# Kernel optimization log

Hardware: AMD Instinct MI355X
Metric: run time of the kernel (lower is better)

## Reference

```python
import jax, jax.numpy as jnp
import numpy as np

B, T, D, H = 2, 2048, 1024, 16
Dh = D // H


def _rope(q, k):
    # q, k: (B, H, T, Dh), interleaved even/odd rotation
    t = q.shape[2]
    dh = q.shape[3]
    inv_freq = 1.0 / (10000.0 ** (jnp.arange(0, dh, 2, dtype=jnp.float32) / dh))
    pos = jnp.arange(t, dtype=jnp.float32)
    freqs = pos[:, None] * inv_freq[None, :]          # (T, Dh/2)
    sin = jnp.sin(freqs)[None, None]                  # (1,1,T,Dh/2)
    cos = jnp.cos(freqs)[None, None]

    def rot(x):
        xe, xo = x[..., ::2], x[..., 1::2]
        re = xe * cos - xo * sin
        ro = xe * sin + xo * cos
        return jnp.stack([re, ro], axis=-1).reshape(x.shape)

    return rot(q), rot(k)


def setup_inputs() -> dict:
    key = jax.random.key(0)
    k1, k2, k3 = jax.random.split(key, 3)
    s = 1.0 / np.sqrt(D)
    return {
        "x": jax.random.normal(k1, (B, T, D), dtype=jnp.float32),
        "w_qkv": jax.random.normal(k2, (3 * D, D), dtype=jnp.float32) * s,
        "b_qkv": jnp.zeros((3 * D,), dtype=jnp.float32),
        "w_out": jax.random.normal(k3, (D, D), dtype=jnp.float32) * s,
        "b_out": jnp.zeros((D,), dtype=jnp.float32),
    }


def reference(x, w_qkv, b_qkv, w_out, b_out):
    b, t, d = x.shape
    qkv = x @ w_qkv.T + b_qkv                         # (B,T,3D)
    q, k, v = jnp.split(qkv, 3, axis=-1)
    q = q.reshape(b, t, H, Dh).transpose(0, 2, 1, 3)  # (B,H,T,Dh)
    k = k.reshape(b, t, H, Dh).transpose(0, 2, 1, 3)
    v = v.reshape(b, t, H, Dh).transpose(0, 2, 1, 3)
    q, k = _rope(q, k)
    scores = jnp.einsum("bhtd,bhsd->bhts", q, k) / jnp.sqrt(jnp.float32(Dh))
    causal = jnp.tril(jnp.ones((t, t), dtype=bool))[None, None]
    scores = jnp.where(causal, scores, -jnp.inf)
    probs = jax.nn.softmax(scores, axis=-1)
    out = jnp.einsum("bhts,bhsd->bhtd", probs, v)     # (B,H,T,Dh)
    out = out.transpose(0, 2, 1, 3).reshape(b, t, d)
    return out @ w_out.T + b_out
```

## Files before the change

kernel.cpp:

```cpp
#include <hip/hip_runtime.h>
#include <hip/hip_bf16.h>
#include <math.h>
#include <type_traits>

#define B_ 2
#define T_ 2048
#define D_ 1024
#define H_ 16
#define DH_ 64

typedef __bf16 bf16_t;
typedef bf16_t bf16x8 __attribute__((ext_vector_type(8)));
typedef bf16_t bf16x4 __attribute__((ext_vector_type(4)));
typedef float f32x4 __attribute__((ext_vector_type(4)));

typedef __attribute__((address_space(1))) const void gas_void;
typedef __attribute__((address_space(3))) void las_void;

__device__ __forceinline__ void gld16(const void* g, void* l) {
    __builtin_amdgcn_global_load_lds((gas_void*)g, (las_void*)l, 16, 0, 0);
}

#define BARRIER() do { asm volatile("" ::: "memory"); __builtin_amdgcn_s_barrier(); asm volatile("" ::: "memory"); } while (0)

__global__ __launch_bounds__(256) void cvt3(const float* __restrict__ a,
                                            const float* __restrict__ b,
                                            const float* __restrict__ c,
                                            bf16_t* __restrict__ oa,
                                            bf16_t* __restrict__ ob,
                                            bf16_t* __restrict__ oc) {
    int i = blockIdx.x * 256 + threadIdx.x;
    const float* src; bf16_t* dst; int off;
    if (i < 1048576)      { src = a; dst = oa; off = i; }
    else if (i < 1835008) { src = b; dst = ob; off = i - 1048576; }
    else                  { src = c; dst = oc; off = i - 1835008; }
    float4 f = ((const float4*)src)[off];
    bf16x4 v = { (bf16_t)f.x, (bf16_t)f.y, (bf16_t)f.z, (bf16_t)f.w };
    ((bf16x4*)dst)[off] = v;
}

__global__ __launch_bounds__(256) void rope_tab_k(float2* __restrict__ tab) {
    int i = blockIdx.x * 256 + threadIdx.x;
    int t = i >> 5, d2 = i & 31;
    float invf = exp2f(-(float)d2 * 0.4152410118609203f);
    float ang = (float)t * invf;
    float sn, cs;
    sincosf(ang, &sn, &cs);
    tab[i] = make_float2(cs, sn);
}

__global__ __launch_bounds__(512, 1) void gemm256qkv(const bf16_t* __restrict__ A,
                                                     const bf16_t* __restrict__ Bw,
                                                     const float* __restrict__ bias,
                                                     const float2* __restrict__ tab,
                                                     bf16_t* __restrict__ q_out,
                                                     bf16_t* __restrict__ k_out,
                                                     bf16_t* __restrict__ vt_out) {
    __shared__ __align__(16) char smem[131072];

    int tid = threadIdx.x;
    int lane = tid & 63, wid = tid >> 6;
    int wm = wid >> 2, wn = wid & 3;
    int lr = lane & 15, lk = lane >> 4;

    int l = blockIdx.y * 12 + blockIdx.x;
    int x = l & 7, c = l >> 3;
    int by = x * 2 + (c >= 12);
    int bx = (c >= 12) ? c - 12 : c;

    f32x4 acc[8][4];
    f32x4 z = {0.f, 0.f, 0.f, 0.f};
#pragma unroll
    for (int i = 0; i < 8; i++)
#pragma unroll
        for (int j = 0; j < 4; j++) acc[i][j] = z;

    int colb = (tid * 16) & 127;
    int rb = tid >> 3;
    int csw = colb ^ ((rb & 7) << 4);
    const char* gA = (const char*)A + (size_t)(by * 256 + rb) * 2048 + csw;
    const char* gB = (const char*)Bw + (size_t)(bx * 256 + rb) * 2048 + csw;

    auto stgA = [&](int par, int h, int kt) __attribute__((always_inline)) {
        char* d = smem + par * 32768 + h * 16384;
        const char* g = gA + (size_t)h * 262144 + kt * 128;
        gld16(g, d + tid * 16);
        gld16(g + 131072, d + 8192 + tid * 16);
    };
    auto stgB = [&](int par, int h, int kt) __attribute__((always_inline)) {
        char* d = smem + 65536 + par * 32768 + h * 16384;
        const char* g = gB + (size_t)h * 262144 + kt * 128;
        gld16(g, d + tid * 16);
        gld16(g + 131072, d + 8192 + tid * 16);
    };

    int swz = (lr & 7) << 4;
    int ca0 = (lk * 16) ^ swz;
    int ca1 = (64 + lk * 16) ^ swz;

    bf16x8 Af[2][2], Bf[4][2];
    auto rdB = [&](const char* cB) __attribute__((always_inline)) {
        const char* base = cB + (wn >> 1) * 16384 + ((wn & 1) * 64) * 128 + lr * 128;
#pragma unroll
        for (int n = 0; n < 4; n++) {
            Bf[n][0] = *(const bf16x8*)(base + n * 2048 + ca0);
            Bf[n][1] = *(const bf16x8*)(base + n * 2048 + ca1);
        }
    };
    auto rdA = [&](const char* cA, int mp) __attribute__((always_inline)) {
        const char* base = cA + wm * 16384 + lr * 128;
#pragma unroll
        for (int mm = 0; mm < 2; mm++) {
            Af[mm][0] = *(const bf16x8*)(base + (mp * 2 + mm) * 2048 + ca0);
            Af[mm][1] = *(const bf16x8*)(base + (mp * 2 + mm) * 2048 + ca1);
        }
    };
    auto mfmaset = [&](int q) __attribute__((always_inline)) {
        __builtin_amdgcn_s_setprio(1);
#pragma unroll
        for (int mm = 0; mm < 2; mm++)
#pragma unroll
            for (int n = 0; n < 4; n++)
#pragma unroll
                for (int ks = 0; ks < 2; ks++)
                    acc[q * 2 + mm][n] = __builtin_amdgcn_mfma_f32_16x16x32_bf16(
                        Af[mm][ks], Bf[n][ks], acc[q * 2 + mm][n], 0, 0, 0);
        __builtin_amdgcn_s_setprio(0);
    };

    stgA(0, 0, 0); stgA(0, 1, 0); stgB(0, 0, 0); stgB(0, 1, 0);

    for (int kt = 0; kt < 15; ++kt) {
        int p = kt & 1, np = p ^ 1;
        const char* cA = smem + p * 32768;
        const char* cB = smem + 65536 + p * 32768;
        stgA(np, 0, kt + 1);
        asm volatile("s_waitcnt vmcnt(2)" ::: "memory");
        BARRIER();
        rdB(cB); rdA(cA, 0); stgA(np, 1, kt + 1);
        BARRIER(); mfmaset(0); BARRIER();
        rdA(cA, 1); stgB(np, 0, kt + 1);
        BARRIER(); mfmaset(1); BARRIER();
        rdA(cA, 2); stgB(np, 1, kt + 1);
        BARRIER(); mfmaset(2); BARRIER();
        rdA(cA, 3);
        BARRIER(); mfmaset(3); BARRIER();
    }
    {
        const char* cA = smem + 32768;
        const char* cB = smem + 65536 + 32768;
        asm volatile("s_waitcnt vmcnt(0)" ::: "memory");
        BARRIER();
        rdB(cB); rdA(cA, 0); BARRIER(); mfmaset(0); BARRIER();
        rdA(cA, 1); BARRIER(); mfmaset(1); BARRIER();
        rdA(cA, 2); BARRIER(); mfmaset(2); BARRIER();
        rdA(cA, 3); BARRIER(); mfmaset(3); BARRIER();
    }

    int m_base = by * 256 + wm * 128;
    int n_base = bx * 256 + wn * 64;
    char* myL = smem + wid * 16384;
    int which = n_base >> 10;
    int h = (n_base & 1023) >> 6;
    int b = m_base >> 11, t0 = m_base & 2047;
    int bh = b * H_ + h;
    if (which == 2) {
#pragma unroll
        for (int m = 0; m < 8; m++)
#pragma unroll
            for (int n = 0; n < 4; n++) {
                int rd = n * 16 + lr;
                float bv = bias[n_base + rd];
#pragma unroll
                for (int j = 0; j < 4; j++) {
                    int ct = m * 16 + lk * 4 + j;
                    int ct2 = (ct & 96) | (((ct >> 2) & 3) << 3) | (((ct >> 4) & 1) << 2) | (ct & 3);
                    int addr = (rd * 256 + ct2 * 2) ^ ((rd & 7) << 4);
                    *(bf16_t*)(myL + addr) = (bf16_t)(acc[m][n][j] + bv);
                }
            }
#pragma unroll
        for (int it = 0; it < 16; it++) {
            int row = it * 4 + (lane >> 4);
            int byt = (lane & 15) * 16;
            bf16x8 val = *(const bf16x8*)(myL + ((row * 256 + byt) ^ ((row & 7) << 4)));
            *(bf16x8*)(vt_out + ((size_t)bh * DH_ + row) * T_ + t0 + (lane & 15) * 8) = val;
        }
    } else {
        bf16_t* dst = which ? k_out : q_out;
        float qscl = which ? 1.0f : 0.18033688011112042f;
#pragma unroll
        for (int m = 0; m < 8; m++)
#pragma unroll
            for (int n = 0; n < 4; n++) {
                int dh = n * 16 + lr;
                float bv = bias[n_base + dh];
                int dh2 = dh >> 1;
                bool even = (dh & 1) == 0;
#pragma unroll
                for (int j = 0; j < 4; j++) {
                    int rt = m * 16 + lk * 4 + j;
                    float v = acc[m][n][j] + bv;
                    float pp = __shfl_xor(v, 1);
                    float2 cs = tab[(t0 + rt) * 32 + dh2];
                    float r = even ? v * cs.x - pp * cs.y : v * cs.x + pp * cs.y;
                    r *= qscl;
                    int addr = (rt * 128 + dh * 2) ^ ((rt & 7) << 4);
                    *(bf16_t*)(myL + addr) = (bf16_t)r;
                }
            }
#pragma unroll
        for (int it = 0; it < 16; it++) {
            int row = it * 8 + (lane >> 3);
            int byt = (lane & 7) * 16;
            bf16x8 val = *(const bf16x8*)(myL + ((row * 128 + byt) ^ ((row & 7) << 4)));
            *(bf16x8*)(dst + ((size_t)bh * T_ + t0 + row) * DH_ + (lane & 7) * 8) = val;
        }
    }
}

__global__ __launch_bounds__(256) void gemm128o(const bf16_t* __restrict__ A,
                                                const bf16_t* __restrict__ Bw,
                                                const float* __restrict__ bias,
                                                float* __restrict__ f_out,
                                                int K, int N) {
    __shared__ __align__(16) char smem[49152];
    char* b0 = smem;
    char* b1 = smem + 16384;
    char* b2 = smem + 32768;

    int tid = threadIdx.x;
    int lane = tid & 63, wid = tid >> 6;
    int wr = wid >> 1, wc = wid & 1;
    int lr = lane & 15, lk = lane >> 4;

    int l = blockIdx.y * gridDim.x + blockIdx.x;
    int chunk = (gridDim.x * gridDim.y) >> 3;
    int u = (l & 7) * chunk + (l >> 3);
    int bx = u % gridDim.x;
    int by = u / gridDim.x;

    f32x4 acc[4][4];
    f32x4 z = {0.f, 0.f, 0.f, 0.f};
#pragma unroll
    for (int i = 0; i < 4; i++)
#pragma unroll
        for (int j = 0; j < 4; j++) acc[i][j] = z;

    const char* Ab = (const char*)(A + (size_t)by * 128 * K);
    const char* Bb = (const char*)(Bw + (size_t)bx * 128 * K);
    const int rowstride = K * 2;

    int p0 = tid * 16;
    int p1 = 4096 + tid * 16;
    int r0 = p0 >> 6, r1 = p1 >> 6;
    int cb0 = (p0 & 63) ^ (((r0 >> 1) & 3) << 4);
    int cb1 = (p1 & 63) ^ (((r1 >> 1) & 3) << 4);
    size_t gA0 = (size_t)r0 * rowstride + cb0;
    size_t gA1 = (size_t)r1 * rowstride + cb1;

    int oa[4], ob[4];
#pragma unroll
    for (int m = 0; m < 4; m++) {
        int row = wr * 64 + m * 16 + lr;
        oa[m] = row * 64 + ((lk * 16) ^ (((row >> 1) & 3) << 4));
    }
#pragma unroll
    for (int n = 0; n < 4; n++) {
        int row = wc * 64 + n * 16 + lr;
        ob[n] = row * 64 + ((lk * 16) ^ (((row >> 1) & 3) << 4));
    }

    auto stg = [&](char* buf, int ks) __attribute__((always_inline)) {
        const char* Ag = Ab + (size_t)ks * 64;
        const char* Bg = Bb + (size_t)ks * 64;
        gld16(Ag + gA0, buf + p0);
        gld16(Ag + gA1, buf + p1);
        gld16(Bg + gA0, buf + 8192 + p0);
        gld16(Bg + gA1, buf + 8192 + p1);
    };

    auto iterf = [&](auto vmc, char* buf, int ks, bool dostage) __attribute__((always_inline)) {
        constexpr int VM = decltype(vmc)::value;
        if constexpr (VM == 8)      asm volatile("s_waitcnt vmcnt(8)" ::: "memory");
        else if constexpr (VM == 4) asm volatile("s_waitcnt vmcnt(4)" ::: "memory");
        else                        asm volatile("s_waitcnt vmcnt(0)" ::: "memory");
        __builtin_amdgcn_s_barrier();
        asm volatile("" ::: "memory");
        bf16x8 Af[4], Bf[4];
#pragma unroll
        for (int m = 0; m < 4; m++) Af[m] = *(const bf16x8*)(buf + oa[m]);
#pragma unroll
        for (int n = 0; n < 4; n++) Bf[n] = *(const bf16x8*)(buf + 8192 + ob[n]);
#pragma unroll
        for (int m = 0; m < 4; m++)
#pragma unroll
            for (int n = 0; n < 4; n++)
                acc[m][n] = __builtin_amdgcn_mfma_f32_16x16x32_bf16(Af[m], Bf[n], acc[m][n], 0, 0, 0);
        asm volatile("" ::: "memory");
        __builtin_amdgcn_s_barrier();
        asm volatile("" ::: "memory");
        if (dostage) stg(buf, ks);
    };

    std::integral_constant<int, 8> c8;
    std::integral_constant<int, 4> c4;
    std::integral_constant<int, 0> c0;

    stg(b0, 0);
    stg(b1, 1);
    stg(b2, 2);
    for (int s = 0; s < 30; s += 3) {
        iterf(c8, b0, s + 3, s + 3 < 32);
        iterf(c8, b1, s + 4, s + 4 < 32);
        iterf(c8, b2, s + 5, s + 5 < 32);
    }
    iterf(c4, b0, 0, false);
    iterf(c0, b1, 0, false);

    int m_base = by * 128 + wr * 64;
    int n_base = bx * 128 + wc * 64;
#pragma unroll
    for (int m = 0; m < 4; m++) {
        int gm0 = m_base + m * 16 + lk * 4;
#pragma unroll
        for (int n = 0; n < 4; n++) {
            int nc = n_base + n * 16 + lr;
            float bv = bias[nc];
#pragma unroll
            for (int j = 0; j < 4; j++)
                f_out[(size_t)(gm0 + j) * N + nc] = acc[m][n][j] + bv;
        }
    }
}

__global__ __launch_bounds__(256, 4) void attn64(const bf16_t* __restrict__ Q,
                                                 const bf16_t* __restrict__ K,
                                                 const bf16_t* __restrict__ Vt,
                                                 bf16_t* __restrict__ Ao) {
    __shared__ __align__(16) char smem[40960];

    int tid = threadIdx.x;
    int lane = tid & 63, wid = tid >> 6;
    int lr = lane & 15, lk = lane >> 4;
    int xcd = blockIdx.x & 7, idx = blockIdx.x >> 3;
    int bh = xcd * 4 + (idx & 3);
    int i5 = idx >> 2;
    int qq = i5 & 7, rr = i5 >> 3;
    int qt = (rr == 0) ? qq : (rr == 1) ? 15 - qq : (rr == 2) ? 16 + qq : 31 - qq;
    int q0 = qt * 64;
    int qrel = wid * 16 + lr;

    const bf16_t* Qp = Q + ((size_t)bh * T_ + q0 + qrel) * DH_;
    bf16x8 qf0 = *(const bf16x8*)(Qp + lk * 8);
    bf16x8 qf1 = *(const bf16x8*)(Qp + 32 + lk * 8);

    f32x4 zz = {0.f, 0.f, 0.f, 0.f};
    f32x4 oacc[4];
#pragma unroll
    for (int dt = 0; dt < 4; dt++) oacc[dt] = zz;
    float mrun = -__builtin_inff(), lsum = 0.f;

    const char* Kbase = (const char*)(K + (size_t)bh * T_ * DH_);
    const char* Vbase = (const char*)(Vt + (size_t)bh * DH_ * T_);

    auto stage = [&](int s, char* Kd, char* Vd) __attribute__((always_inline)) {
        int kv0 = s * 64;
        const char* Kg = Kbase + (size_t)kv0 * 128;
#pragma unroll
        for (int c = 0; c < 2; c++) {
            int o = c * 4096 + tid * 16;
            int r = o >> 7;
            int g = o ^ ((r & 7) << 4);
            gld16(Kg + g, Kd + o);
            gld16(Vbase + (size_t)r * (T_ * 2) + kv0 * 2 + (g & 127), Vd + o);
        }
    };

    float p[4][4];
    bf16x8 pb0, pb1;

    auto do_qk = [&](const char* Kc, auto dmc) __attribute__((always_inline)) {
        constexpr bool DM = decltype(dmc)::value;
#pragma unroll
        for (int kt = 0; kt < 4; kt++) {
            int row = kt * 16 + lr;
            int key = (row & 7) << 4;
            bf16x8 kf0 = *(const bf16x8*)(Kc + ((row * 128 + lk * 16) ^ key));
            bf16x8 kf1 = *(const bf16x8*)(Kc + ((row * 128 + 64 + lk * 16) ^ key));
            f32x4 sacc = zz;
            sacc = __builtin_amdgcn_mfma_f32_16x16x32_bf16(kf0, qf0, sacc, 0, 0, 0);
            sacc = __builtin_amdgcn_mfma_f32_16x16x32_bf16(kf1, qf1, sacc, 0, 0, 0);
#pragma unroll
            for (int j = 0; j < 4; j++) {
                if (DM) {
                    int kvrel = kt * 16 + lk * 4 + j;
                    p[kt][j] = (kvrel <= qrel) ? sacc[j] : -__builtin_inff();
                } else {
                    p[kt][j] = sacc[j];
                }
            }
        }
    };

    auto do_pv = [&](const char* Vc) __attribute__((always_inline)) {
#pragma unroll
        for (int dt = 0; dt < 4; dt++) {
            int row = dt * 16 + lr;
            int key = (row & 7) << 4;
            bf16x8 vf0 = *(const bf16x8*)(Vc + ((row * 128 + lk * 16) ^ key));
            bf16x8 vf1 = *(const bf16x8*)(Vc + ((row * 128 + 64 + lk * 16) ^ key));
            f32x4 o = oacc[dt];
            o = __builtin_amdgcn_mfma_f32_16x16x32_bf16(vf0, pb0, o, 0, 0, 0);
            o = __builtin_amdgcn_mfma_f32_16x16x32_bf16(vf1, pb1, o, 0, 0, 0);
            oacc[dt] = o;
        }
    };

    auto do_softmax = [&]() __attribute__((always_inline)) {
        float mk[4];
#pragma unroll
        for (int kt = 0; kt < 4; kt++)
            mk[kt] = fmaxf(fmaxf(p[kt][0], p[kt][1]), fmaxf(p[kt][2], p[kt][3]));
        float mx = fmaxf(fmaxf(mk[0], mk[1]), fmaxf(mk[2], mk[3]));
        mx = fmaxf(mx, __shfl_xor(mx, 16));
        mx = fmaxf(mx, __shfl_xor(mx, 32));
        if (!__all(mx <= mrun + 8.f)) {
            float mnew = fmaxf(mrun, mx);
            float fac = exp2f(mrun - mnew);
            mrun = mnew;
            lsum *= fac;
#pragma unroll
            for (int dt = 0; dt < 4; dt++) oacc[dt] = oacc[dt] * fac;
        }
        float rs = 0.f;
#pragma unroll
        for (int kt = 0; kt < 4; kt++)
#pragma unroll
            for (int j = 0; j < 4; j++) {
                float e = exp2f(p[kt][j] - mrun);
                p[kt][j] = e;
                rs += e;
            }
        rs += __shfl_xor(rs, 16);
        rs += __shfl_xor(rs, 32);
        lsum += rs;
        pb0 = bf16x8{ (bf16_t)p[0][0], (bf16_t)p[0][1], (bf16_t)p[0][2], (bf16_t)p[0][3],
                      (bf16_t)p[1][0], (bf16_t)p[1][1], (bf16_t)p[1][2], (bf16_t)p[1][3] };
        pb1 = bf16x8{ (bf16_t)p[2][0], (bf16_t)p[2][1], (bf16_t)p[2][2], (bf16_t)p[2][3],
                      (bf16_t)p[3][0], (bf16_t)p[3][1], (bf16_t)p[3][2], (bf16_t)p[3][3] };
    };

    std::integral_constant<bool, true>  mask_y;
    std::integral_constant<bool, false> mask_n;

    stage(0, smem, smem + 16384);
    stage(1, smem + 8192, smem + 24576);
    asm volatile("s_waitcnt vmcnt(4)" ::: "memory");
    __builtin_amdgcn_s_barrier();
    asm volatile("" ::: "memory");
    if (qt == 0) do_qk(smem, mask_y); else do_qk(smem, mask_n);
    do_softmax();

    char* Kr = smem + 8192;
    char* Kw = smem;
    char* Vr = smem + 16384;
    char* Vn = smem + 24576;
    char* Vw = smem + 32768;

    auto iter = [&](int s, auto dmc) __attribute__((always_inline)) {
        asm volatile("s_waitcnt vmcnt(0)" ::: "memory");
        __builtin_amdgcn_s_barrier();
        asm volatile("" ::: "memory");
        if (s + 2 <= qt) stage(s + 2, Kw, Vw);
        do_qk(Kr, dmc);
        do_pv(Vr);
        do_softmax();
        char* t;
        t = Kr; Kr = Kw; Kw = t;
        t = Vr; Vr = Vn; Vn = Vw; Vw = t;
    };

    for (int s = 0; s + 1 < qt; ++s) iter(s, mask_n);
    if (qt > 0) iter(qt - 1, mask_y);
    do_pv(Vr);
    __syncthreads();

    char* myL = smem + wid * 2048;
    float rinv = __builtin_amdgcn_rcpf(lsum);
#pragma unroll
    for (int dt = 0; dt < 4; dt++)
#pragma unroll
        for (int j = 0; j < 4; j++) {
            int dh = dt * 16 + lk * 4 + j;
            int addr = (lr * 128 + dh * 2) ^ ((lr & 7) << 4);
            *(bf16_t*)(myL + addr) = (bf16_t)(oacc[dt][j] * rinv);
        }
    int b = bh >> 4, h = bh & 15;
#pragma unroll
    for (int it = 0; it < 2; it++) {
        int row = it * 8 + (lane >> 3);
        int byt = (lane & 7) * 16;
        bf16x8 val = *(const bf16x8*)(myL + ((row * 128 + byt) ^ ((row & 7) << 4)));
        int t = q0 + wid * 16 + row;
        *(bf16x8*)(Ao + ((size_t)b * T_ + t) * D_ + h * DH_ + (lane & 7) * 8) = val;
    }
}

extern "C" void kernel_launch(void* const* d_in, const int* in_sizes, int n_in,
                              void* d_out, int out_size, void* d_ws, size_t ws_size,
                              hipStream_t stream) {
    const float* x     = (const float*)d_in[0];
    const float* w_qkv = (const float*)d_in[1];
    const float* b_qkv = (const float*)d_in[2];
    const float* w_out = (const float*)d_in[3];
    const float* b_out = (const float*)d_in[4];
    float* out = (float*)d_out;

    char* ws = (char*)d_ws;
    bf16_t* xb    = (bf16_t*)(ws);
    bf16_t* wqkvb = (bf16_t*)(ws + 8388608);
    bf16_t* wob   = (bf16_t*)(ws + 14680064);
    bf16_t* qb    = (bf16_t*)(ws + 16777216);
    bf16_t* kb    = (bf16_t*)(ws + 25165824);
    bf16_t* vtb   = (bf16_t*)(ws + 33554432);
    bf16_t* ab    = (bf16_t*)(ws + 41943040);
    float2* tab   = (float2*)(ws + 41943040);

    rope_tab_k<<<256, 256, 0, stream>>>(tab);
    cvt3<<<8192, 256, 0, stream>>>(x, w_qkv, w_out, xb, wqkvb, wob);

    gemm256qkv<<<dim3(12, 16), 512, 0, stream>>>(xb, wqkvb, b_qkv, tab, qb, kb, vtb);
    attn64<<<1024, 256, 0, stream>>>(qb, kb, vtb, ab);
    gemm128o<<<dim3(8, 32), 256, 0, stream>>>(ab, wob, b_out, out, 1024, 1024);
}
```

Baseline: 114.5 us.

## Fuse RoPE table into convert kernel and restructure QKV GEMM main loop

Folds the RoPE sin/cos table generation into the bf16 conversion kernel as extra blocks, which removes one kernel launch. Rewrites the QKV GEMM K-loop to use a single vmcnt(0) wait and one barrier per k-tile, plus a guarded final iteration, instead of many barriers around each MFMA group. This is meant to cut barrier stalls and let loads overlap with MFMAs. It also changes launch_bounds to 2 blocks per CU. With 128 fp32 accumulators per thread, that register cap risks spills, and the 128KB LDS footprint likely prevents a second block from fitting anyway.

```diff
diff --git a/kernel.cpp b/kernel.cpp
--- a/kernel.cpp
+++ b/kernel.cpp
@@ -28,7 +28,18 @@
                                             const float* __restrict__ c,
                                             bf16_t* __restrict__ oa,
                                             bf16_t* __restrict__ ob,
-                                            bf16_t* __restrict__ oc) {
+                                            bf16_t* __restrict__ oc,
+                                            float2* __restrict__ tab) {
+    if (blockIdx.x >= 8192) {
+        int j = (blockIdx.x - 8192) * 256 + threadIdx.x;
+        int t = j >> 5, d2 = j & 31;
+        float invf = exp2f(-(float)d2 * 0.4152410118609203f);
+        float ang = (float)t * invf;
+        float sn, cs;
+        sincosf(ang, &sn, &cs);
+        tab[j] = make_float2(cs, sn);
+        return;
+    }
     int i = blockIdx.x * 256 + threadIdx.x;
     const float* src; bf16_t* dst; int off;
     if (i < 1048576)      { src = a; dst = oa; off = i; }
@@ -39,17 +50,7 @@
     ((bf16x4*)dst)[off] = v;
 }
 
-__global__ __launch_bounds__(256) void rope_tab_k(float2* __restrict__ tab) {
-    int i = blockIdx.x * 256 + threadIdx.x;
-    int t = i >> 5, d2 = i & 31;
-    float invf = exp2f(-(float)d2 * 0.4152410118609203f);
-    float ang = (float)t * invf;
-    float sn, cs;
-    sincosf(ang, &sn, &cs);
-    tab[i] = make_float2(cs, sn);
-}
-
-__global__ __launch_bounds__(512, 1) void gemm256qkv(const bf16_t* __restrict__ A,
+__global__ __launch_bounds__(512, 2) void gemm256qkv(const bf16_t* __restrict__ A,
                                                      const bf16_t* __restrict__ Bw,
                                                      const float* __restrict__ bias,
                                                      const float2* __restrict__ tab,
@@ -130,32 +131,27 @@
 
     stgA(0, 0, 0); stgA(0, 1, 0); stgB(0, 0, 0); stgB(0, 1, 0);
 
-    for (int kt = 0; kt < 15; ++kt) {
+    for (int kt = 0; kt < 16; ++kt) {
         int p = kt & 1, np = p ^ 1;
         const char* cA = smem + p * 32768;
         const char* cB = smem + 65536 + p * 32768;
-        stgA(np, 0, kt + 1);
-        asm volatile("s_waitcnt vmcnt(2)" ::: "memory");
-        BARRIER();
-        rdB(cB); rdA(cA, 0); stgA(np, 1, kt + 1);
-        BARRIER(); mfmaset(0); BARRIER();
-        rdA(cA, 1); stgB(np, 0, kt + 1);
-        BARRIER(); mfmaset(1); BARRIER();
-        rdA(cA, 2); stgB(np, 1, kt + 1);
-        BARRIER(); mfmaset(2); BARRIER();
-        rdA(cA, 3);
-        BARRIER(); mfmaset(3); BARRIER();
-    }
-    {
-        const char* cA = smem + 32768;
-        const char* cB = smem + 65536 + 32768;
         asm volatile("s_waitcnt vmcnt(0)" ::: "memory");
         BARRIER();
-        rdB(cB); rdA(cA, 0); BARRIER(); mfmaset(0); BARRIER();
-        rdA(cA, 1); BARRIER(); mfmaset(1); BARRIER();
-        rdA(cA, 2); BARRIER(); mfmaset(2); BARRIER();
-        rdA(cA, 3); BARRIER(); mfmaset(3); BARRIER();
-    }
+        bool st = kt < 15;
+        rdB(cB);
+        if (st) { stgA(np, 0, kt + 1); stgA(np, 1, kt + 1); }
+        rdA(cA, 0);
+        if (st) stgB(np, 0, kt + 1);
+        mfmaset(0);
+        rdA(cA, 1);
+        if (st) stgB(np, 1, kt + 1);
+        mfmaset(1);
+        rdA(cA, 2);
+        mfmaset(2);
+        rdA(cA, 3);
+        mfmaset(3);
+    }
+    BARRIER();
 
     int m_base = by * 256 + wm * 128;
     int n_base = bx * 256 + wn * 64;
@@ -527,8 +523,7 @@
     bf16_t* ab    = (bf16_t*)(ws + 41943040);
     float2* tab   = (float2*)(ws + 41943040);
 
-    rope_tab_k<<<256, 256, 0, stream>>>(tab);
-    cvt3<<<8192, 256, 0, stream>>>(x, w_qkv, w_out, xb, wqkvb, wob);
+    cvt3<<<8448, 256, 0, stream>>>(x, w_qkv, w_out, xb, wqkvb, wob, tab);
 
     gemm256qkv<<<dim3(12, 16), 512, 0, stream>>>(xb, wqkvb, b_qkv, tab, qb, kb, vtb);
     attn64<<<1024, 256, 0, stream>>>(qb, kb, vtb, ab);
```

New measurement: 107.1 us. 1.07x faster.
